# Kernel optimization log

Hardware: AMD Instinct MI355X
Metric: run time of the kernel (lower is better)

The kernel has to match this reference:

```python
import jax, jax.numpy as jnp
import numpy as np

N = 2048       # num_nodes
D = 256        # node_embedding_dim
E = 16         # edge_embedding_dim
H = 8          # heads
QK = 32        # query_key_dim = D // H
V = 32         # value_dim
OUT = 256      # out_dim


def setup_inputs() -> dict:
    key = jax.random.key(0)
    ks = jax.random.split(key, 8)

    def xavier(k, shape, fan_in, fan_out):
        std = float(np.sqrt(2.0 / (fan_in + fan_out)))
        return jax.random.normal(k, shape, dtype=jnp.float32) * std

    return {
        "edge_embeddings": jax.random.normal(ks[0], (N, N, E), dtype=jnp.float32),
        "node_embeddings": jax.random.normal(ks[1], (N, D), dtype=jnp.float32),
        "query_tensor": xavier(ks[2], (H, D, QK), D, QK),
        "node_key_tensor": xavier(ks[3], (H, D, QK), D, QK),
        "edge_key_tensor": xavier(ks[4], (E, QK), E, QK),
        "node_value_tensor": xavier(ks[5], (H, D, V), D, V),
        "edge_value_tensor": xavier(ks[6], (E, V), E, V),
        "output_tensor": xavier(ks[7], (H, V, OUT), V, OUT),
    }


def reference(edge_embeddings, node_embeddings, query_tensor, node_key_tensor,
              edge_key_tensor, node_value_tensor, edge_value_tensor,
              output_tensor):
    qk_dim = query_tensor.shape[-1]

    # Queries and keys per head: [h, n, q]
    query = jnp.einsum('nd,hdq->hnq', node_embeddings, query_tensor)
    node_key = jnp.einsum('md,hdq->hmq', node_embeddings, node_key_tensor)
    # Node-node dot-product logits: [h, n, m]
    dot_product_logits = jnp.einsum('hmq,hnq->hnm', node_key, query)

    # RAT-style edge keys (shared across heads): [n, m, q]
    edge_key = jnp.einsum('nme,eq->nmq', edge_embeddings, edge_key_tensor)
    edge_logits = jnp.einsum('nmq,hnq->hnm', edge_key, query)

    attention_logits = (dot_product_logits + edge_logits) / jnp.sqrt(
        jnp.asarray(qk_dim, dtype=node_embeddings.dtype))
    attention_weights = jax.nn.softmax(attention_logits, axis=2)  # [h, n, m]

    # Node values: [h, m, v] -> weighted sum [h, n, v]
    node_value = jnp.einsum('md,hdv->hmv', node_embeddings, node_value_tensor)
    attention_node_value = jnp.einsum('hnm,hmv->hnv', attention_weights,
                                      node_value)

    # Edge values (shared across heads): [n, m, v] -> weighted sum [h, n, v]
    edge_value = jnp.einsum('nme,ev->nmv', edge_embeddings, edge_value_tensor)
    attention_edge_value = jnp.einsum('hnm,nmv->hnv', attention_weights,
                                      edge_value)

    attention_value = attention_node_value + attention_edge_value
    # Output projection: [n, out]
    return jnp.einsum('hnv,hvo->no', attention_value, output_tensor)
```

## Files before the change

kernel.cpp:

```cpp
#include <hip/hip_runtime.h>
#include <hip/hip_bf16.h>

typedef unsigned short u16;
typedef unsigned int u32;
typedef __attribute__((ext_vector_type(8))) short bf16x8;
typedef __attribute__((ext_vector_type(4))) float f32x4;

#define NN 2048
#define DM 256
#define ED 16
#define HH 8
#define QK 32
#define VV 32
#define OUTD 256

#define LBAR() asm volatile("s_waitcnt lgkmcnt(0)\n\ts_barrier" ::: "memory")

__device__ __forceinline__ u16 f2bf(float f) {
    __hip_bfloat16 h = __float2bfloat16(f);
    return *reinterpret_cast<u16*>(&h);
}
__device__ __forceinline__ u32 cvt2(float a, float b) {
    __hip_bfloat162 h = __float22bfloat162_rn(make_float2(a, b));
    return *reinterpret_cast<u32*>(&h);
}

__global__ __launch_bounds__(256) void k1_precompute(
    const float* __restrict__ node_g, const float* __restrict__ qt_g,
    const float* __restrict__ nkt_g, const float* __restrict__ nvt_g,
    const float* __restrict__ ek_g,
    u16* __restrict__ qbf, u16* __restrict__ qebf,
    u16* __restrict__ nk_ws, u16* __restrict__ nvT_ws) {
    __shared__ __align__(16) float node_s[32][256];
    __shared__ __align__(16) float qtmp_s[32][32];
    const int t = threadIdx.x;
    const int h = blockIdx.x >> 6;
    const int n0 = (blockIdx.x & 63) * 32;
#pragma unroll
    for (int c = 0; c < 8; ++c) {
        const int ci = t + c * 256;
        const int nl = ci >> 6, d4 = ci & 63;
        *(float4*)&node_s[nl][d4 * 4] =
            *(const float4*)&node_g[(size_t)(n0 + nl) * 256 + d4 * 4];
    }
    __syncthreads();
    const int q = t & 31, nb = t >> 5;
    const float scale = 0.17677669529663689f;

#define PROJ_LOOP(Wp, STORE0, STORE1, STORE2, STORE3)                          \
    {                                                                          \
        const float* W = Wp;                                                   \
        float a0 = 0.f, a1 = 0.f, a2 = 0.f, a3 = 0.f;                          \
        for (int d4 = 0; d4 < 64; ++d4) {                                      \
            const float w0 = W[(d4 * 4 + 0) * 32 + q];                         \
            const float w1 = W[(d4 * 4 + 1) * 32 + q];                         \
            const float w2 = W[(d4 * 4 + 2) * 32 + q];                         \
            const float w3 = W[(d4 * 4 + 3) * 32 + q];                         \
            float4 nd;                                                         \
            nd = *(const float4*)&node_s[nb][d4 * 4];                          \
            a0 += nd.x * w0 + nd.y * w1 + nd.z * w2 + nd.w * w3;               \
            nd = *(const float4*)&node_s[nb + 8][d4 * 4];                      \
            a1 += nd.x * w0 + nd.y * w1 + nd.z * w2 + nd.w * w3;               \
            nd = *(const float4*)&node_s[nb + 16][d4 * 4];                     \
            a2 += nd.x * w0 + nd.y * w1 + nd.z * w2 + nd.w * w3;               \
            nd = *(const float4*)&node_s[nb + 24][d4 * 4];                     \
            a3 += nd.x * w0 + nd.y * w1 + nd.z * w2 + nd.w * w3;               \
        }                                                                      \
        STORE0; STORE1; STORE2; STORE3;                                        \
    }

    PROJ_LOOP(qt_g + h * (DM * QK),
        { float v = a0 * scale; qtmp_s[nb][q] = v;      qbf[((size_t)h * NN + n0 + nb) * 32 + q] = f2bf(v); },
        { float v = a1 * scale; qtmp_s[nb + 8][q] = v;  qbf[((size_t)h * NN + n0 + nb + 8) * 32 + q] = f2bf(v); },
        { float v = a2 * scale; qtmp_s[nb + 16][q] = v; qbf[((size_t)h * NN + n0 + nb + 16) * 32 + q] = f2bf(v); },
        { float v = a3 * scale; qtmp_s[nb + 24][q] = v; qbf[((size_t)h * NN + n0 + nb + 24) * 32 + q] = f2bf(v); })
    PROJ_LOOP(nkt_g + h * (DM * QK),
        { nk_ws[((size_t)h * NN + n0 + nb) * 32 + q] = f2bf(a0); },
        { nk_ws[((size_t)h * NN + n0 + nb + 8) * 32 + q] = f2bf(a1); },
        { nk_ws[((size_t)h * NN + n0 + nb + 16) * 32 + q] = f2bf(a2); },
        { nk_ws[((size_t)h * NN + n0 + nb + 24) * 32 + q] = f2bf(a3); })
    PROJ_LOOP(nvt_g + h * (DM * QK),
        { nvT_ws[((size_t)h * 32 + q) * NN + n0 + nb] = f2bf(a0); },
        { nvT_ws[((size_t)h * 32 + q) * NN + n0 + nb + 8] = f2bf(a1); },
        { nvT_ws[((size_t)h * 32 + q) * NN + n0 + nb + 16] = f2bf(a2); },
        { nvT_ws[((size_t)h * 32 + q) * NN + n0 + nb + 24] = f2bf(a3); })
#undef PROJ_LOOP
    __syncthreads();
#pragma unroll
    for (int c = 0; c < 2; ++c) {
        const int idx = t + c * 256;
        const int nl = idx >> 4, e = idx & 15;
        float s = 0.f;
#pragma unroll
        for (int qq = 0; qq < 32; ++qq) s = fmaf(qtmp_s[nl][qq], ek_g[e * 32 + qq], s);
        qebf[((size_t)h * NN + n0 + nl) * 16 + e] = f2bf(s);
    }
}

__global__ __launch_bounds__(512, 4) void k2_attn(
    const float* __restrict__ ee_g, const u16* __restrict__ qbf,
    const u16* __restrict__ qebf, const u16* __restrict__ nk_g,
    const u16* __restrict__ nvT_g, float* __restrict__ accv_ws,
    float* __restrict__ acce_ws, float* __restrict__ ml_ws) {
    __shared__ __align__(16) u16 ee_s[2][16 * 520];
    __shared__ __align__(16) u16 eeT_s[16 * 640];
    __shared__ __align__(16) float el_s[16 * 260];
    __shared__ __align__(16) u16 p_s[16 * 264];
    __shared__ float a_s[16 * 8];

    const int t = threadIdx.x;
    const int w = t >> 6;
    const int l = t & 63;
    const int col = l & 15;
    const int g = l >> 4;
    const int h = w;
    const int nt = blockIdx.x >> 2;
    const int ck = blockIdx.x & 3;
    const int n0 = nt * 16;
    const int mbase = ck * 512;
    const int sn = t >> 5, sj = (t >> 1) & 15, seh = t & 1;

    const bf16x8 Qfrag = *(const bf16x8*)&qbf[((size_t)h * NN + n0 + col) * 32 + 8 * g];
    bf16x8 qeA[2];
#pragma unroll
    for (int s2 = 0; s2 < 2; ++s2) {
        bf16x8 z = {0, 0, 0, 0, 0, 0, 0, 0};
        if (col < 8 && g < 2)
            z = *(const bf16x8*)&qebf[((size_t)col * NN + n0 + 2 * w + s2) * 16 + 8 * g];
        qeA[s2] = z;
    }

    f32x4 accpv0 = {0.f, 0.f, 0.f, 0.f}, accpv1 = {0.f, 0.f, 0.f, 0.f};
    f32x4 acce0 = {0.f, 0.f, 0.f, 0.f}, acce1 = {0.f, 0.f, 0.f, 0.f};
    float M = -INFINITY, Ls = 0.f;

    float4 r0, r1, r2, r3;
    {
        const float* src = ee_g + ((size_t)(n0 + sn) * NN + mbase + 2 * sj) * 16 + seh * 8;
        r0 = *(const float4*)(src);
        r1 = *(const float4*)(src + 4);
        r2 = *(const float4*)(src + 16);
        r3 = *(const float4*)(src + 20);
        *(uint4*)&ee_s[0][sn * 520 + (2 * sj) * 16 + seh * 8] =
            make_uint4(cvt2(r0.x, r0.y), cvt2(r0.z, r0.w), cvt2(r1.x, r1.y), cvt2(r1.z, r1.w));
        *(uint4*)&ee_s[0][sn * 520 + (2 * sj + 1) * 16 + seh * 8] =
            make_uint4(cvt2(r2.x, r2.y), cvt2(r2.z, r2.w), cvt2(r3.x, r3.y), cvt2(r3.z, r3.w));
    }
    LBAR();

    const f32x4 zf = {0.f, 0.f, 0.f, 0.f};

#pragma unroll 1
    for (int it = 0; it < 16; ++it) {
        const int m0 = mbase + it * 32;
        const u16* eeb = ee_s[it & 1];

        {
            u32* dstT = (u32*)&eeT_s[sn * 640 + (seh * 8) * 40 + 2 * sj];
            dstT[0 * 20] = cvt2(r0.x, r2.x);
            dstT[1 * 20] = cvt2(r0.y, r2.y);
            dstT[2 * 20] = cvt2(r0.z, r2.z);
            dstT[3 * 20] = cvt2(r0.w, r2.w);
            dstT[4 * 20] = cvt2(r1.x, r3.x);
            dstT[5 * 20] = cvt2(r1.y, r3.y);
            dstT[6 * 20] = cvt2(r1.z, r3.z);
            dstT[7 * 20] = cvt2(r1.w, r3.w);
        }

        if (it < 15) {
            const float* src = ee_g + ((size_t)(n0 + sn) * NN + m0 + 32 + 2 * sj) * 16 + seh * 8;
            r0 = *(const float4*)(src);
            r1 = *(const float4*)(src + 4);
            r2 = *(const float4*)(src + 16);
            r3 = *(const float4*)(src + 20);
        }

        f32x4 sn0, sn1;
        {
            const bf16x8 Kf0 = *(const bf16x8*)&nk_g[((size_t)h * NN + m0 + col) * 32 + 8 * g];
            const bf16x8 Kf1 = *(const bf16x8*)&nk_g[((size_t)h * NN + m0 + 16 + col) * 32 + 8 * g];
            sn0 = __builtin_amdgcn_mfma_f32_16x16x32_bf16(Kf0, Qfrag, zf, 0, 0, 0);
            sn1 = __builtin_amdgcn_mfma_f32_16x16x32_bf16(Kf1, Qfrag, zf, 0, 0, 0);
        }

#pragma unroll
        for (int s2 = 0; s2 < 2; ++s2) {
            const int nsl = 2 * w + s2;
#pragma unroll
            for (int s = 0; s < 2; ++s) {
                bf16x8 Bf = {0, 0, 0, 0, 0, 0, 0, 0};
                if (g < 2)
                    Bf = *(const bf16x8*)&eeb[nsl * 520 + (s * 16 + col) * 16 + 8 * g];
                f32x4 d = __builtin_amdgcn_mfma_f32_16x16x32_bf16(qeA[s2], Bf, zf, 0, 0, 0);
                if (l < 32) {
#pragma unroll
                    for (int reg = 0; reg < 4; ++reg)
                        el_s[nsl * 260 + (4 * g + reg) * 32 + s * 16 + col] = d[reg];
                }
            }
        }
        LBAR();

        {
            const float4 e0 = *(const float4*)&el_s[col * 260 + h * 32 + 4 * g];
            const float4 e1 = *(const float4*)&el_s[col * 260 + h * 32 + 16 + 4 * g];
            float lv[8];
            lv[0] = sn0[0] + e0.x; lv[1] = sn0[1] + e0.y;
            lv[2] = sn0[2] + e0.z; lv[3] = sn0[3] + e0.w;
            lv[4] = sn1[0] + e1.x; lv[5] = sn1[1] + e1.y;
            lv[6] = sn1[2] + e1.z; lv[7] = sn1[3] + e1.w;
            float tm = fmaxf(fmaxf(fmaxf(lv[0], lv[1]), fmaxf(lv[2], lv[3])),
                             fmaxf(fmaxf(lv[4], lv[5]), fmaxf(lv[6], lv[7])));
            tm = fmaxf(tm, __shfl_xor(tm, 16));
            tm = fmaxf(tm, __shfl_xor(tm, 32));
            const float nM = fmaxf(M, tm);
            const float a = __expf(M - nM);
            M = nM;
            Ls *= a;
#pragma unroll
            for (int r = 0; r < 4; ++r) { accpv0[r] *= a; accpv1[r] *= a; }
            float p[8];
#pragma unroll
            for (int i = 0; i < 8; ++i) { p[i] = __expf(lv[i] - nM); Ls += p[i]; }
            uint2 pk0, pk1;
            pk0.x = cvt2(p[0], p[1]); pk0.y = cvt2(p[2], p[3]);
            pk1.x = cvt2(p[4], p[5]); pk1.y = cvt2(p[6], p[7]);
            *(uint2*)&p_s[col * 264 + h * 32 + 4 * g] = pk0;
            *(uint2*)&p_s[col * 264 + h * 32 + 16 + 4 * g] = pk1;
            if (l < 16) a_s[col * 8 + h] = a;
        }
        LBAR();

        {
            const bf16x8 Pf = *(const bf16x8*)&p_s[col * 264 + h * 32 + 8 * g];
            const bf16x8 Vf0 = *(const bf16x8*)&nvT_g[((size_t)h * 32 + col) * NN + m0 + 8 * g];
            const bf16x8 Vf1 = *(const bf16x8*)&nvT_g[((size_t)h * 32 + 16 + col) * NN + m0 + 8 * g];
            accpv0 = __builtin_amdgcn_mfma_f32_16x16x32_bf16(Vf0, Pf, accpv0, 0, 0, 0);
            accpv1 = __builtin_amdgcn_mfma_f32_16x16x32_bf16(Vf1, Pf, accpv1, 0, 0, 0);
        }

        {
            const bf16x8 Pn0 = *(const bf16x8*)&p_s[(2 * w + 0) * 264 + (col & 7) * 32 + 8 * g];
            const bf16x8 Pn1 = *(const bf16x8*)&p_s[(2 * w + 1) * 264 + (col & 7) * 32 + 8 * g];
            const bf16x8 B0 = *(const bf16x8*)&eeT_s[(2 * w + 0) * 640 + col * 40 + 8 * g];
            const bf16x8 B1 = *(const bf16x8*)&eeT_s[(2 * w + 1) * 640 + col * 40 + 8 * g];
            const float4 av0 = *(const float4*)&a_s[(2 * w + 0) * 8 + ((4 * g) & 7)];
            const float4 av1 = *(const float4*)&a_s[(2 * w + 1) * 8 + ((4 * g) & 7)];
            acce0[0] *= av0.x; acce0[1] *= av0.y; acce0[2] *= av0.z; acce0[3] *= av0.w;
            acce1[0] *= av1.x; acce1[1] *= av1.y; acce1[2] *= av1.z; acce1[3] *= av1.w;
            acce0 = __builtin_amdgcn_mfma_f32_16x16x32_bf16(Pn0, B0, acce0, 0, 0, 0);
            acce1 = __builtin_amdgcn_mfma_f32_16x16x32_bf16(Pn1, B1, acce1, 0, 0, 0);
        }

        if (it < 15) {
            u16* dst = (u16*)ee_s[(it + 1) & 1];
            *(uint4*)&dst[sn * 520 + (2 * sj) * 16 + seh * 8] =
                make_uint4(cvt2(r0.x, r0.y), cvt2(r0.z, r0.w), cvt2(r1.x, r1.y), cvt2(r1.z, r1.w));
            *(uint4*)&dst[sn * 520 + (2 * sj + 1) * 16 + seh * 8] =
                make_uint4(cvt2(r2.x, r2.y), cvt2(r2.z, r2.w), cvt2(r3.x, r3.y), cvt2(r3.z, r3.w));
        }
        LBAR();
    }

    Ls += __shfl_xor(Ls, 16);
    Ls += __shfl_xor(Ls, 32);

    {
        float* avp = accv_ws + (((size_t)ck * 8 + h) * NN + n0 + col) * 32;
#pragma unroll
        for (int reg = 0; reg < 4; ++reg) {
            avp[4 * g + reg] = accpv0[reg];
            avp[16 + 4 * g + reg] = accpv1[reg];
        }
    }
    if (l < 32) {
#pragma unroll
        for (int s2 = 0; s2 < 2; ++s2) {
            const f32x4 acc = (s2 == 0) ? acce0 : acce1;
#pragma unroll
            for (int reg = 0; reg < 4; ++reg) {
                const int hr = 4 * g + reg;
                acce_ws[(((size_t)ck * 8 + hr) * NN + n0 + 2 * w + s2) * 16 + col] = acc[reg];
            }
        }
    }
    if (l < 16) {
        float* mlp = ml_ws + (((size_t)ck * 8 + h) * NN + n0 + col) * 2;
        mlp[0] = M;
        mlp[1] = Ls;
    }
}

__global__ __launch_bounds__(256) void k3_combine(
    const float* __restrict__ accv_ws, const float* __restrict__ acce_ws,
    const float* __restrict__ ml_ws, const float* __restrict__ ev_g,
    const float* __restrict__ ot_g, float* __restrict__ out_g) {
    __shared__ float w_s[64][4];
    __shared__ float ae_s[8 * 8 * 16];
    __shared__ __align__(16) float av_s[256 * 8];
    const int t = threadIdx.x;
    const int n0 = blockIdx.x * 8;
    if (t < 64) {
        const int h = t >> 3, nl = t & 7, gn = n0 + nl;
        float Mc[4], Lc[4];
#pragma unroll
        for (int c = 0; c < 4; ++c) {
            Mc[c] = ml_ws[(((size_t)c * 8 + h) * NN + gn) * 2 + 0];
            Lc[c] = ml_ws[(((size_t)c * 8 + h) * NN + gn) * 2 + 1];
        }
        float Mx = fmaxf(fmaxf(Mc[0], Mc[1]), fmaxf(Mc[2], Mc[3]));
        float ex[4], den = 0.f;
#pragma unroll
        for (int c = 0; c < 4; ++c) { ex[c] = __expf(Mc[c] - Mx); den += ex[c] * Lc[c]; }
        const float inv = 1.0f / den;
#pragma unroll
        for (int c = 0; c < 4; ++c) w_s[t][c] = ex[c] * inv;
    }
    __syncthreads();
#pragma unroll
    for (int c2 = 0; c2 < 4; ++c2) {
        const int idx = t + c2 * 256;
        const int nl = idx >> 7, h = (idx >> 4) & 7, e = idx & 15;
        const int gn = n0 + nl;
        float s = 0.f;
#pragma unroll
        for (int c = 0; c < 4; ++c)
            s += w_s[h * 8 + nl][c] * acce_ws[(((size_t)c * 8 + h) * NN + gn) * 16 + e];
        ae_s[(nl * 8 + h) * 16 + e] = s;
    }
    __syncthreads();
#pragma unroll
    for (int c2 = 0; c2 < 8; ++c2) {
        const int idx = t + c2 * 256;
        const int nl = idx >> 8, h = (idx >> 5) & 7, v = idx & 31;
        const int gn = n0 + nl;
        float x = 0.f;
#pragma unroll
        for (int c = 0; c < 4; ++c)
            x += w_s[h * 8 + nl][c] * accv_ws[(((size_t)c * 8 + h) * NN + gn) * 32 + v];
        const float* aep = &ae_s[(nl * 8 + h) * 16];
#pragma unroll
        for (int e = 0; e < 16; ++e) x = fmaf(aep[e], ev_g[e * 32 + v], x);
        av_s[(h * 32 + v) * 8 + nl] = x;
    }
    __syncthreads();
    {
        const int o = t;
        float r0 = 0, r1 = 0, r2 = 0, r3 = 0, r4 = 0, r5 = 0, r6 = 0, r7 = 0;
#pragma unroll 4
        for (int k = 0; k < 256; ++k) {
            const float w = ot_g[k * 256 + o];
            const float* av = &av_s[k * 8];
            r0 = fmaf(av[0], w, r0); r1 = fmaf(av[1], w, r1);
            r2 = fmaf(av[2], w, r2); r3 = fmaf(av[3], w, r3);
            r4 = fmaf(av[4], w, r4); r5 = fmaf(av[5], w, r5);
            r6 = fmaf(av[6], w, r6); r7 = fmaf(av[7], w, r7);
        }
        out_g[(size_t)(n0 + 0) * 256 + o] = r0;
        out_g[(size_t)(n0 + 1) * 256 + o] = r1;
        out_g[(size_t)(n0 + 2) * 256 + o] = r2;
        out_g[(size_t)(n0 + 3) * 256 + o] = r3;
        out_g[(size_t)(n0 + 4) * 256 + o] = r4;
        out_g[(size_t)(n0 + 5) * 256 + o] = r5;
        out_g[(size_t)(n0 + 6) * 256 + o] = r6;
        out_g[(size_t)(n0 + 7) * 256 + o] = r7;
    }
}

extern "C" void kernel_launch(void* const* d_in, const int* in_sizes, int n_in,
                              void* d_out, int out_size, void* d_ws, size_t ws_size,
                              hipStream_t stream) {
    (void)in_sizes; (void)n_in; (void)out_size; (void)ws_size;
    const float* ee = (const float*)d_in[0];
    const float* node = (const float*)d_in[1];
    const float* qt = (const float*)d_in[2];
    const float* nkt = (const float*)d_in[3];
    const float* ek = (const float*)d_in[4];
    const float* nvt = (const float*)d_in[5];
    const float* ev = (const float*)d_in[6];
    const float* ot = (const float*)d_in[7];
    float* out = (float*)d_out;

    char* ws = (char*)d_ws;
    u16* qbf = (u16*)(ws);
    u16* qebf = (u16*)(ws + (1u << 20));
    u16* nk_ws = (u16*)(ws + (1u << 20) + (1u << 19));
    u16* nvT_ws = (u16*)(ws + (2u << 20) + (1u << 19));
    float* accv_ws = (float*)(ws + (3u << 20) + (1u << 19));
    float* acce_ws = (float*)(ws + (11u << 20) + (1u << 19));
    float* ml_ws = (float*)(ws + (15u << 20) + (1u << 19));

    hipLaunchKernelGGL(k1_precompute, dim3(512), dim3(256), 0, stream,
                       node, qt, nkt, nvt, ek, qbf, qebf, nk_ws, nvT_ws);
    hipLaunchKernelGGL(k2_attn, dim3(512), dim3(512), 0, stream,
                       ee, qbf, qebf, nk_ws, nvT_ws, accv_ws, acce_ws, ml_ws);
    hipLaunchKernelGGL(k3_combine, dim3(256), dim3(256), 0, stream,
                       accv_ws, acce_ws, ml_ws, ev, ot, out);
}
```

Baseline: 151.9 us.

## Restructure attention loop barriers, prefetch K/V fragments, use exp2 with folded log2e

```diff
diff --git a/kernel.cpp b/kernel.cpp
--- a/kernel.cpp
+++ b/kernel.cpp
@@ -16,6 +16,7 @@
 
 #define LBAR() asm volatile("s_waitcnt lgkmcnt(0)\n\ts_barrier" ::: "memory")
 
+__device__ __forceinline__ float fexp2(float x) { return __builtin_amdgcn_exp2f(x); }
 __device__ __forceinline__ u16 f2bf(float f) {
     __hip_bfloat16 h = __float2bfloat16(f);
     return *reinterpret_cast<u16*>(&h);
@@ -45,7 +46,7 @@
     }
     __syncthreads();
     const int q = t & 31, nb = t >> 5;
-    const float scale = 0.17677669529663689f;
+    const float scale = 0.17677669529663689f * 1.4426950408889634f;
 
 #define PROJ_LOOP(Wp, STORE0, STORE1, STORE2, STORE3)                          \
     {                                                                          \
@@ -102,8 +103,8 @@
     const u16* __restrict__ qebf, const u16* __restrict__ nk_g,
     const u16* __restrict__ nvT_g, float* __restrict__ accv_ws,
     float* __restrict__ acce_ws, float* __restrict__ ml_ws) {
-    __shared__ __align__(16) u16 ee_s[2][16 * 520];
-    __shared__ __align__(16) u16 eeT_s[16 * 640];
+    __shared__ __align__(16) u16 ee_s[16 * 520];
+    __shared__ __align__(16) u16 eeT_s[2][16 * 576];
     __shared__ __align__(16) float el_s[16 * 260];
     __shared__ __align__(16) u16 p_s[16 * 264];
     __shared__ float a_s[16 * 8];
@@ -135,15 +136,20 @@
     float M = -INFINITY, Ls = 0.f;
 
     float4 r0, r1, r2, r3;
+    bf16x8 Kf0, Kf1, Vf0, Vf1;
     {
         const float* src = ee_g + ((size_t)(n0 + sn) * NN + mbase + 2 * sj) * 16 + seh * 8;
         r0 = *(const float4*)(src);
         r1 = *(const float4*)(src + 4);
         r2 = *(const float4*)(src + 16);
         r3 = *(const float4*)(src + 20);
-        *(uint4*)&ee_s[0][sn * 520 + (2 * sj) * 16 + seh * 8] =
+        Kf0 = *(const bf16x8*)&nk_g[((size_t)h * NN + mbase + col) * 32 + 8 * g];
+        Kf1 = *(const bf16x8*)&nk_g[((size_t)h * NN + mbase + 16 + col) * 32 + 8 * g];
+        Vf0 = *(const bf16x8*)&nvT_g[((size_t)h * 32 + col) * NN + mbase + 8 * g];
+        Vf1 = *(const bf16x8*)&nvT_g[((size_t)h * 32 + 16 + col) * NN + mbase + 8 * g];
+        *(uint4*)&ee_s[sn * 520 + (2 * sj) * 16 + seh * 8] =
             make_uint4(cvt2(r0.x, r0.y), cvt2(r0.z, r0.w), cvt2(r1.x, r1.y), cvt2(r1.z, r1.w));
-        *(uint4*)&ee_s[0][sn * 520 + (2 * sj + 1) * 16 + seh * 8] =
+        *(uint4*)&ee_s[sn * 520 + (2 * sj + 1) * 16 + seh * 8] =
             make_uint4(cvt2(r2.x, r2.y), cvt2(r2.z, r2.w), cvt2(r3.x, r3.y), cvt2(r3.z, r3.w));
     }
     LBAR();
@@ -153,20 +159,18 @@
 #pragma unroll 1
     for (int it = 0; it < 16; ++it) {
         const int m0 = mbase + it * 32;
-        const u16* eeb = ee_s[it & 1];
 
         {
-            u32* dstT = (u32*)&eeT_s[sn * 640 + (seh * 8) * 40 + 2 * sj];
-            dstT[0 * 20] = cvt2(r0.x, r2.x);
-            dstT[1 * 20] = cvt2(r0.y, r2.y);
-            dstT[2 * 20] = cvt2(r0.z, r2.z);
-            dstT[3 * 20] = cvt2(r0.w, r2.w);
-            dstT[4 * 20] = cvt2(r1.x, r3.x);
-            dstT[5 * 20] = cvt2(r1.y, r3.y);
-            dstT[6 * 20] = cvt2(r1.z, r3.z);
-            dstT[7 * 20] = cvt2(r1.w, r3.w);
-        }
-
+            u32* dstT = (u32*)&eeT_s[it & 1][0] + sn * 288 + seh * 144 + sj;
+            dstT[0 * 18] = cvt2(r0.x, r2.x);
+            dstT[1 * 18] = cvt2(r0.y, r2.y);
+            dstT[2 * 18] = cvt2(r0.z, r2.z);
+            dstT[3 * 18] = cvt2(r0.w, r2.w);
+            dstT[4 * 18] = cvt2(r1.x, r3.x);
+            dstT[5 * 18] = cvt2(r1.y, r3.y);
+            dstT[6 * 18] = cvt2(r1.z, r3.z);
+            dstT[7 * 18] = cvt2(r1.w, r3.w);
+        }
         if (it < 15) {
             const float* src = ee_g + ((size_t)(n0 + sn) * NN + m0 + 32 + 2 * sj) * 16 + seh * 8;
             r0 = *(const float4*)(src);
@@ -174,15 +178,8 @@
             r2 = *(const float4*)(src + 16);
             r3 = *(const float4*)(src + 20);
         }
-
-        f32x4 sn0, sn1;
-        {
-            const bf16x8 Kf0 = *(const bf16x8*)&nk_g[((size_t)h * NN + m0 + col) * 32 + 8 * g];
-            const bf16x8 Kf1 = *(const bf16x8*)&nk_g[((size_t)h * NN + m0 + 16 + col) * 32 + 8 * g];
-            sn0 = __builtin_amdgcn_mfma_f32_16x16x32_bf16(Kf0, Qfrag, zf, 0, 0, 0);
-            sn1 = __builtin_amdgcn_mfma_f32_16x16x32_bf16(Kf1, Qfrag, zf, 0, 0, 0);
-        }
-
+        f32x4 sn0 = __builtin_amdgcn_mfma_f32_16x16x32_bf16(Kf0, Qfrag, zf, 0, 0, 0);
+        f32x4 sn1 = __builtin_amdgcn_mfma_f32_16x16x32_bf16(Kf1, Qfrag, zf, 0, 0, 0);
 #pragma unroll
         for (int s2 = 0; s2 < 2; ++s2) {
             const int nsl = 2 * w + s2;
@@ -190,38 +187,36 @@
             for (int s = 0; s < 2; ++s) {
                 bf16x8 Bf = {0, 0, 0, 0, 0, 0, 0, 0};
                 if (g < 2)
-                    Bf = *(const bf16x8*)&eeb[nsl * 520 + (s * 16 + col) * 16 + 8 * g];
+                    Bf = *(const bf16x8*)&ee_s[nsl * 520 + (s * 16 + col) * 16 + 8 * g];
                 f32x4 d = __builtin_amdgcn_mfma_f32_16x16x32_bf16(qeA[s2], Bf, zf, 0, 0, 0);
-                if (l < 32) {
-#pragma unroll
-                    for (int reg = 0; reg < 4; ++reg)
-                        el_s[nsl * 260 + (4 * g + reg) * 32 + s * 16 + col] = d[reg];
-                }
+                if (l < 32)
+                    *(float4*)&el_s[nsl * 260 + (s * 16 + col) * 8 + 4 * g] =
+                        make_float4(d[0], d[1], d[2], d[3]);
             }
         }
         LBAR();
 
         {
-            const float4 e0 = *(const float4*)&el_s[col * 260 + h * 32 + 4 * g];
-            const float4 e1 = *(const float4*)&el_s[col * 260 + h * 32 + 16 + 4 * g];
+            const float* elp = &el_s[col * 260 + h];
             float lv[8];
-            lv[0] = sn0[0] + e0.x; lv[1] = sn0[1] + e0.y;
-            lv[2] = sn0[2] + e0.z; lv[3] = sn0[3] + e0.w;
-            lv[4] = sn1[0] + e1.x; lv[5] = sn1[1] + e1.y;
-            lv[6] = sn1[2] + e1.z; lv[7] = sn1[3] + e1.w;
+#pragma unroll
+            for (int r = 0; r < 4; ++r) {
+                lv[r]     = sn0[r] + elp[(4 * g + r) * 8];
+                lv[4 + r] = sn1[r] + elp[(16 + 4 * g + r) * 8];
+            }
             float tm = fmaxf(fmaxf(fmaxf(lv[0], lv[1]), fmaxf(lv[2], lv[3])),
                              fmaxf(fmaxf(lv[4], lv[5]), fmaxf(lv[6], lv[7])));
             tm = fmaxf(tm, __shfl_xor(tm, 16));
             tm = fmaxf(tm, __shfl_xor(tm, 32));
             const float nM = fmaxf(M, tm);
-            const float a = __expf(M - nM);
+            const float a = fexp2(M - nM);
             M = nM;
             Ls *= a;
 #pragma unroll
             for (int r = 0; r < 4; ++r) { accpv0[r] *= a; accpv1[r] *= a; }
             float p[8];
 #pragma unroll
-            for (int i = 0; i < 8; ++i) { p[i] = __expf(lv[i] - nM); Ls += p[i]; }
+            for (int i = 0; i < 8; ++i) { p[i] = fexp2(lv[i] - nM); Ls += p[i]; }
             uint2 pk0, pk1;
             pk0.x = cvt2(p[0], p[1]); pk0.y = cvt2(p[2], p[3]);
             pk1.x = cvt2(p[4], p[5]); pk1.y = cvt2(p[6], p[7]);
@@ -229,21 +224,24 @@
             *(uint2*)&p_s[col * 264 + h * 32 + 16 + 4 * g] = pk1;
             if (l < 16) a_s[col * 8 + h] = a;
         }
-        LBAR();
-
         {
             const bf16x8 Pf = *(const bf16x8*)&p_s[col * 264 + h * 32 + 8 * g];
-            const bf16x8 Vf0 = *(const bf16x8*)&nvT_g[((size_t)h * 32 + col) * NN + m0 + 8 * g];
-            const bf16x8 Vf1 = *(const bf16x8*)&nvT_g[((size_t)h * 32 + 16 + col) * NN + m0 + 8 * g];
             accpv0 = __builtin_amdgcn_mfma_f32_16x16x32_bf16(Vf0, Pf, accpv0, 0, 0, 0);
             accpv1 = __builtin_amdgcn_mfma_f32_16x16x32_bf16(Vf1, Pf, accpv1, 0, 0, 0);
         }
+        if (it < 15) {
+            *(uint4*)&ee_s[sn * 520 + (2 * sj) * 16 + seh * 8] =
+                make_uint4(cvt2(r0.x, r0.y), cvt2(r0.z, r0.w), cvt2(r1.x, r1.y), cvt2(r1.z, r1.w));
+            *(uint4*)&ee_s[sn * 520 + (2 * sj + 1) * 16 + seh * 8] =
+                make_uint4(cvt2(r2.x, r2.y), cvt2(r2.z, r2.w), cvt2(r3.x, r3.y), cvt2(r3.z, r3.w));
+        }
+        LBAR();
 
         {
             const bf16x8 Pn0 = *(const bf16x8*)&p_s[(2 * w + 0) * 264 + (col & 7) * 32 + 8 * g];
             const bf16x8 Pn1 = *(const bf16x8*)&p_s[(2 * w + 1) * 264 + (col & 7) * 32 + 8 * g];
-            const bf16x8 B0 = *(const bf16x8*)&eeT_s[(2 * w + 0) * 640 + col * 40 + 8 * g];
-            const bf16x8 B1 = *(const bf16x8*)&eeT_s[(2 * w + 1) * 640 + col * 40 + 8 * g];
+            const bf16x8 B0 = *(const bf16x8*)&eeT_s[it & 1][(2 * w + 0) * 576 + col * 36 + 8 * g];
+            const bf16x8 B1 = *(const bf16x8*)&eeT_s[it & 1][(2 * w + 1) * 576 + col * 36 + 8 * g];
             const float4 av0 = *(const float4*)&a_s[(2 * w + 0) * 8 + ((4 * g) & 7)];
             const float4 av1 = *(const float4*)&a_s[(2 * w + 1) * 8 + ((4 * g) & 7)];
             acce0[0] *= av0.x; acce0[1] *= av0.y; acce0[2] *= av0.z; acce0[3] *= av0.w;
@@ -251,15 +249,12 @@
             acce0 = __builtin_amdgcn_mfma_f32_16x16x32_bf16(Pn0, B0, acce0, 0, 0, 0);
             acce1 = __builtin_amdgcn_mfma_f32_16x16x32_bf16(Pn1, B1, acce1, 0, 0, 0);
         }
-
         if (it < 15) {
-            u16* dst = (u16*)ee_s[(it + 1) & 1];
-            *(uint4*)&dst[sn * 520 + (2 * sj) * 16 + seh * 8] =
-                make_uint4(cvt2(r0.x, r0.y), cvt2(r0.z, r0.w), cvt2(r1.x, r1.y), cvt2(r1.z, r1.w));
-            *(uint4*)&dst[sn * 520 + (2 * sj + 1) * 16 + seh * 8] =
-                make_uint4(cvt2(r2.x, r2.y), cvt2(r2.z, r2.w), cvt2(r3.x, r3.y), cvt2(r3.z, r3.w));
-        }
-        LBAR();
+            Kf0 = *(const bf16x8*)&nk_g[((size_t)h * NN + m0 + 32 + col) * 32 + 8 * g];
+            Kf1 = *(const bf16x8*)&nk_g[((size_t)h * NN + m0 + 48 + col) * 32 + 8 * g];
+            Vf0 = *(const bf16x8*)&nvT_g[((size_t)h * 32 + col) * NN + m0 + 32 + 8 * g];
+            Vf1 = *(const bf16x8*)&nvT_g[((size_t)h * 32 + 16 + col) * NN + m0 + 32 + 8 * g];
+        }
     }
 
     Ls += __shfl_xor(Ls, 16);
@@ -311,7 +306,7 @@
         float Mx = fmaxf(fmaxf(Mc[0], Mc[1]), fmaxf(Mc[2], Mc[3]));
         float ex[4], den = 0.f;
 #pragma unroll
-        for (int c = 0; c < 4; ++c) { ex[c] = __expf(Mc[c] - Mx); den += ex[c] * Lc[c]; }
+        for (int c = 0; c < 4; ++c) { ex[c] = __builtin_amdgcn_exp2f(Mc[c] - Mx); den += ex[c] * Lc[c]; }
         const float inv = 1.0f / den;
 #pragma unroll
         for (int c = 0; c < 4; ++c) w_s[t][c] = ex[c] * inv;
```

Result: faster. 143.4 us (-5.6%).
